# Optimization experiments

Measured on AMD Instinct MI355X. Metric: run time of the kernel, lower is better.

## Reference

```python
import jax, jax.numpy as jnp
import numpy as np

NUM_HEADS = 16
WINDOW = 16  # hard-coded in module; half-window = 8


def sliding_mask(seq_len):
    # mask[i, j] = 0 if j in [i - W//2, i + W//2], else -inf  (additive)
    i = jnp.arange(seq_len)[:, None]
    j = jnp.arange(seq_len)[None, :]
    return jnp.where(jnp.abs(i - j) <= WINDOW // 2, 0.0, -jnp.inf).astype(jnp.float32)


def setup_inputs() -> dict:
    key = jax.random.key(0)
    k1, k2, k3 = jax.random.split(key, 3)
    B, S, D = 2, 2048, 1024
    scale = 1.0 / np.sqrt(D)
    return {
        "input_embeddings": jax.random.normal(k1, (B, S, D), dtype=jnp.float32),
        "token_ids": jax.random.randint(k2, (B, S), 0, 32000, dtype=jnp.int64),
        # nn.MultiheadAttention params: packed in_proj [3D, D] + bias, out_proj [D, D] + bias
        "w_qkv": jax.random.normal(jax.random.fold_in(k3, 0), (3 * D, D), dtype=jnp.float32) * scale,
        "b_qkv": jnp.zeros((3 * D,), dtype=jnp.float32),
        "w_out": jax.random.normal(jax.random.fold_in(k3, 1), (D, D), dtype=jnp.float32) * scale,
        "b_out": jnp.zeros((D,), dtype=jnp.float32),
    }


def reference(input_embeddings, token_ids, w_qkv, b_qkv, w_out, b_out):
    B, S, D = input_embeddings.shape
    H = NUM_HEADS
    hd = D // H
    # packed QKV projection (torch in_proj): [B, S, 3D]
    qkv = input_embeddings @ w_qkv.T + b_qkv
    q, k, v = jnp.split(qkv, 3, axis=-1)
    # [B, H, S, hd]
    q = q.reshape(B, S, H, hd).transpose(0, 2, 1, 3)
    k = k.reshape(B, S, H, hd).transpose(0, 2, 1, 3)
    v = v.reshape(B, S, H, hd).transpose(0, 2, 1, 3)
    scores = jnp.einsum("bhqd,bhkd->bhqk", q, k) / jnp.sqrt(jnp.asarray(hd, q.dtype))
    scores = scores + sliding_mask(S)  # broadcast additive [S, S] mask
    attn = jax.nn.softmax(scores, axis=-1)
    ctx = jnp.einsum("bhqk,bhkd->bhqd", attn, v)
    ctx = ctx.transpose(0, 2, 1, 3).reshape(B, S, D)
    return ctx @ w_out.T + b_out
```

## Files before the change

### kernel.cpp

```cpp
#include <hip/hip_runtime.h>
#include <stdint.h>


typedef __bf16 bf16_t;
typedef bf16_t bf16x8 __attribute__((ext_vector_type(8)));
typedef unsigned short u16x8 __attribute__((ext_vector_type(8)));
typedef float f32x4 __attribute__((ext_vector_type(4)));

#define GLD16(g, l)                                                        \
  __builtin_amdgcn_global_load_lds(                                        \
      (const __attribute__((address_space(1))) void*)(g),                  \
      (__attribute__((address_space(3))) void*)(l), 16, 0, 0)

__device__ __forceinline__ unsigned short f2bf(float f) {
  unsigned int u = __float_as_uint(f);
  u += 0x7FFFu + ((u >> 16) & 1u);
  return (unsigned short)(u >> 16);
}

__device__ __forceinline__ bf16x8 ld16(const unsigned short* p) {
  return __builtin_bit_cast(bf16x8, *reinterpret_cast<const u16x8*>(p));
}

__global__ void cvt_all(const float* __restrict__ x, const float* __restrict__ wq,
                        const float* __restrict__ wo, unsigned short* __restrict__ xb,
                        unsigned short* __restrict__ wqb,
                        unsigned short* __restrict__ wob) {
  const int N0 = 1048576, N1 = 786432, N2 = 262144;
  for (int i = blockIdx.x * blockDim.x + threadIdx.x; i < N0 + N1 + N2;
       i += gridDim.x * blockDim.x) {
    const float4* src;
    unsigned short* dst;
    int j;
    if (i < N0) { src = (const float4*)x; dst = xb; j = i; }
    else if (i < N0 + N1) { src = (const float4*)wq; dst = wqb; j = i - N0; }
    else { src = (const float4*)wo; dst = wob; j = i - N0 - N1; }
    const float4 f = src[j];
    ushort4 o;
    o.x = f2bf(f.x); o.y = f2bf(f.y); o.z = f2bf(f.z); o.w = f2bf(f.w);
    reinterpret_cast<ushort4*>(dst)[j] = o;
  }
}

template <int EPI>
__global__ __launch_bounds__(256, 2) void gemm_bt(
    const unsigned short* __restrict__ A,
    const unsigned short* __restrict__ Bt,
    const float* __restrict__ bias,
    unsigned short* __restrict__ Cq, unsigned short* __restrict__ Ck,
    unsigned short* __restrict__ Cv, float* __restrict__ Cp, int M, int N,
    int K, int gny) {
  __shared__ unsigned short sA[2][8192];
  __shared__ unsigned short sB[2][8192];

  const int tid = threadIdx.x;
  const int wave = tid >> 6;
  const int lane = tid & 63;

  const int nwg = gridDim.x;
  const int bid = blockIdx.x;
  const int cw = (nwg >> 3) / gny;
  const int xcd = bid & 7;
  const int idx = bid >> 3;
  const int m0 = (xcd * cw + idx % cw) * 128;
  const int n0 = (idx / cw) * 128;

  const int wr = wave >> 1;
  const int wc = wave & 1;

  f32x4 acc[4][4] = {};

  const int srow = (wave << 3) + (lane >> 3);
  const int sslot = ((lane & 7) ^ (lane >> 3)) << 3;
  const unsigned short* Ag = A + (size_t)(m0 + srow) * K + sslot;
  const unsigned short* Bg = Bt + (size_t)(n0 + srow) * K + sslot;
  const int wdst = wave * 512;

  const int T = K >> 6;

  auto stage = [&](int t, int b) {
#pragma unroll
    for (int r = 0; r < 4; ++r) {
      GLD16(Ag + (size_t)(r * 32) * K + t * 64, &sA[b][r * 2048 + wdst]);
      GLD16(Bg + (size_t)(r * 32) * K + t * 64, &sB[b][r * 2048 + wdst]);
    }
  };

  stage(0, 0);
  stage(1, 1);

  const int kg = lane >> 4;
  const int l7 = lane & 7;
  const int arr = wr * 64 + (lane & 15);
  const int brr = wc * 64 + (lane & 15);

  for (int t = 0; t < T; ++t) {
    if (t < T - 1)
      asm volatile("s_waitcnt vmcnt(8)" ::: "memory");
    else
      asm volatile("s_waitcnt vmcnt(0)" ::: "memory");
    __builtin_amdgcn_s_barrier();

    const int b = t & 1;
    const unsigned short* sAb = sA[b];
    const unsigned short* sBb = sB[b];
    bf16x8 af[2][4], bfr[2][4];
#pragma unroll
    for (int st = 0; st < 2; ++st) {
#pragma unroll
      for (int f = 0; f < 4; ++f) {
        const int se = ((st << 2) | kg) ^ l7;
        af[st][f] = ld16(&sAb[(arr + f * 16) * 64 + (se << 3)]);
        bfr[st][f] = ld16(&sBb[(brr + f * 16) * 64 + (se << 3)]);
      }
    }
    asm volatile("s_waitcnt lgkmcnt(0)" ::: "memory");
    __builtin_amdgcn_sched_barrier(0);
    __builtin_amdgcn_s_barrier();

    if (t + 2 < T) stage(t + 2, b);

#pragma unroll
    for (int st = 0; st < 2; ++st)
#pragma unroll
      for (int i = 0; i < 4; ++i)
#pragma unroll
        for (int j = 0; j < 4; ++j)
          acc[i][j] = __builtin_amdgcn_mfma_f32_16x16x32_bf16(
              af[st][i], bfr[st][j], acc[i][j], 0, 0, 0);
  }

#pragma unroll
  for (int i = 0; i < 4; ++i) {
    const int row0 = m0 + wr * 64 + i * 16 + ((lane >> 4) << 2);
#pragma unroll
    for (int j = 0; j < 4; ++j) {
      const int col = n0 + wc * 64 + j * 16 + (lane & 15);
      const float bb = bias[col];
#pragma unroll
      for (int r = 0; r < 4; ++r) {
        const int m = row0 + r;
        const float val = acc[i][j][r] + bb;
        if (EPI == 0) {
          Cp[(size_t)m * N + col] = val;
        } else {
          const int b2 = m >> 11, s = m & 2047;
          const int which = col >> 10, nn = col & 1023;
          const int h = nn >> 6, d = nn & 63;
          const int bh = (b2 << 4) + h;
          const unsigned short vb = f2bf(val);
          if (which == 0)
            Cq[((size_t)(bh * 2048 + s)) * 64 + d] = vb;
          else if (which == 1)
            Ck[((size_t)(bh * 2048 + s)) * 64 + d] = vb;
          else
            Cv[((size_t)(bh * 64 + d)) * 2048 + s] = vb;
        }
      }
    }
  }
}

__global__ __launch_bounds__(256) void attn_mfma(
    const unsigned short* __restrict__ Qb, const unsigned short* __restrict__ Kb,
    const unsigned short* __restrict__ Vt, unsigned short* __restrict__ ctx) {
  __shared__ unsigned short P[4][16][40];
  const int wave = threadIdx.x >> 6;
  const int lane = threadIdx.x & 63;
  const int gw = (blockIdx.x << 2) + wave;
  const int bh = gw >> 7;
  const int i0 = (gw & 127) << 4;
  const int qr = lane & 15;
  const int kg = lane >> 4;
  const int kc = kg << 3;

  const size_t qbase = ((size_t)(bh * 2048 + i0 + qr)) * 64;
  const bf16x8 aq0 = ld16(Qb + qbase + kc);
  const bf16x8 aq1 = ld16(Qb + qbase + 32 + kc);

  f32x4 sc0 = {0.f, 0.f, 0.f, 0.f}, sc1 = {0.f, 0.f, 0.f, 0.f};
  {
    const int ka0 = i0 - 8 + qr;
    const int ka1 = ka0 + 16;
    const int kcl0 = min(max(ka0, 0), 2047);
    const int kcl1 = min(max(ka1, 0), 2047);
    const unsigned short* K0 = Kb + ((size_t)(bh * 2048 + kcl0)) * 64;
    const unsigned short* K1 = Kb + ((size_t)(bh * 2048 + kcl1)) * 64;
    sc0 = __builtin_amdgcn_mfma_f32_16x16x32_bf16(aq0, ld16(K0 + kc), sc0, 0, 0, 0);
    sc0 = __builtin_amdgcn_mfma_f32_16x16x32_bf16(aq1, ld16(K0 + 32 + kc), sc0, 0, 0, 0);
    sc1 = __builtin_amdgcn_mfma_f32_16x16x32_bf16(aq0, ld16(K1 + kc), sc1, 0, 0, 0);
    sc1 = __builtin_amdgcn_mfma_f32_16x16x32_bf16(aq1, ld16(K1 + 32 + kc), sc1, 0, 0, 0);
  }

  unsigned short* Pw = &P[wave][0][0];
  float lsum[4];
#pragma unroll
  for (int r = 0; r < 4; ++r) {
    const int q = (kg << 2) + r;
    const int key0 = qr, key1 = 16 + qr;
    const int ka0 = i0 - 8 + key0, ka1 = i0 - 8 + key1;
    const bool v0 = (q <= key0) && (key0 <= q + 16) && (ka0 >= 0) && (ka0 < 2048);
    const bool v1 = (q <= key1) && (key1 <= q + 16) && (ka1 >= 0) && (ka1 < 2048);
    const float e0 = v0 ? __expf(sc0[r] * 0.125f) : 0.f;
    const float e1 = v1 ? __expf(sc1[r] * 0.125f) : 0.f;
    Pw[q * 40 + key0] = f2bf(e0);
    Pw[q * 40 + key1] = f2bf(e1);
    float s = e0 + e1;
#pragma unroll
    for (int off = 1; off < 16; off <<= 1) s += __shfl_xor(s, off);
    lsum[r] = s;
  }

  const bf16x8 pa = ld16(&Pw[qr * 40 + kc]);

  const int base_s = min(max(i0 - 8 + kc, 0), 2040);
  f32x4 o[4];
  const f32x4 zero = {0.f, 0.f, 0.f, 0.f};
#pragma unroll
  for (int t2 = 0; t2 < 4; ++t2) {
    const unsigned short* Vr =
        Vt + ((size_t)(bh * 64 + t2 * 16 + qr)) * 2048 + base_s;
    o[t2] = __builtin_amdgcn_mfma_f32_16x16x32_bf16(pa, ld16(Vr), zero, 0, 0, 0);
  }

  const int b = bh >> 4, h = bh & 15;
  float rinv[4];
#pragma unroll
  for (int r = 0; r < 4; ++r) rinv[r] = 1.0f / lsum[r];
#pragma unroll
  for (int t2 = 0; t2 < 4; ++t2) {
#pragma unroll
    for (int r = 0; r < 4; ++r) {
      const int q = (kg << 2) + r;
      const int d = t2 * 16 + qr;
      ctx[((size_t)(b * 2048 + i0 + q)) * 1024 + (h << 6) + d] =
          f2bf(o[t2][r] * rinv[r]);
    }
  }
}

extern "C" void kernel_launch(void* const* d_in, const int* in_sizes, int n_in,
                              void* d_out, int out_size, void* d_ws,
                              size_t ws_size, hipStream_t stream) {
  const float* x = (const float*)d_in[0];
  const float* w_qkv = (const float*)d_in[2];
  const float* b_qkv = (const float*)d_in[3];
  const float* w_out = (const float*)d_in[4];
  const float* b_out = (const float*)d_in[5];
  float* out = (float*)d_out;

  char* ws = (char*)d_ws;
  unsigned short* xb    = (unsigned short*)(ws + 0);
  unsigned short* wqkvb = (unsigned short*)(ws + 8388608);
  unsigned short* woutb = (unsigned short*)(ws + 14680064);
  unsigned short* Qb    = (unsigned short*)(ws + 16777216);
  unsigned short* Kb    = (unsigned short*)(ws + 25165824);
  unsigned short* Vt    = (unsigned short*)(ws + 33554432);
  unsigned short* ctxb  = (unsigned short*)(ws + 41943040);

  cvt_all<<<2048, 256, 0, stream>>>(x, w_qkv, w_out, xb, wqkvb, woutb);

  gemm_bt<1><<<768, 256, 0, stream>>>(xb, wqkvb, b_qkv, Qb, Kb, Vt, nullptr,
                                      4096, 3072, 1024, 24);

  attn_mfma<<<1024, 256, 0, stream>>>(Qb, Kb, Vt, ctxb);

  gemm_bt<0><<<256, 256, 0, stream>>>(ctxb, woutb, b_out, nullptr, nullptr,
                                      nullptr, out, 4096, 1024, 1024, 8);
}
```

Measured before the change: 80.62 us.

## Replace QKV GEMM with 256x256-tile 512-thread kernel with prioritized MFMA

Adds a dedicated QKV projection kernel that uses 256x256 output tiles, 8 waves per block, and a double-buffered LDS pipeline built on direct global-to-LDS loads and explicit waitcnt/barrier scheduling. Each wave computes a 128x64 sub-tile, which raises arithmetic intensity per LDS byte, and s_setprio wraps the MFMA bursts. The generic gemm_bt is left as the fp32 output projection only. The cost is 192 blocks on a 256-CU device, so some CUs sit idle, plus 128 KB of LDS per block and much higher register pressure, which limits occupancy.

```diff
diff --git a/kernel.cpp b/kernel.cpp
--- a/kernel.cpp
+++ b/kernel.cpp
@@ -42,14 +42,137 @@
   }
 }
 
-template <int EPI>
+__global__ __launch_bounds__(512, 2) void gemm256_qkv(
+    const unsigned short* __restrict__ A,
+    const unsigned short* __restrict__ Bt,
+    const float* __restrict__ bias,
+    unsigned short* __restrict__ Cq, unsigned short* __restrict__ Ck,
+    unsigned short* __restrict__ Cv) {
+  __shared__ unsigned short sA[2][16384];
+  __shared__ unsigned short sB[2][16384];
+
+  const int K = 1024;
+  const int tid = threadIdx.x;
+  const int wave = tid >> 6;
+  const int lane = tid & 63;
+  const int bid = blockIdx.x;
+  const int m0 = (bid & 15) << 8;
+  const int n0 = (bid >> 4) << 8;
+
+  const int wr = wave >> 2;
+  const int wc = wave & 3;
+
+  f32x4 acc[8][4] = {};
+
+  const int srow8 = (wave << 3) + (lane >> 3);
+  const int sslot = ((lane & 7) ^ (lane >> 3)) << 3;
+  const unsigned short* Ag = A + (size_t)(m0 + srow8) * K + sslot;
+  const unsigned short* Bg = Bt + (size_t)(n0 + srow8) * K + sslot;
+  const int wdst = wave * 512;
+
+  const int T = 16;
+
+  auto stage = [&](int t, int b) {
+#pragma unroll
+    for (int h = 0; h < 2; ++h)
+#pragma unroll
+      for (int r = 0; r < 2; ++r) {
+        const size_t go = (size_t)(h * 128 + r * 64) * K + t * 64;
+        const int lo = h * 8192 + r * 4096 + wdst;
+        GLD16(Ag + go, &sA[b][lo]);
+        GLD16(Bg + go, &sB[b][lo]);
+      }
+  };
+
+  stage(0, 0);
+  stage(1, 1);
+
+  const int kg = lane >> 4;
+  const int l7 = lane & 7;
+  const int a0 = wr * 8192 + (lane & 15) * 64 + ((kg ^ l7) << 3);
+  const int b0 =
+      (wc >> 1) * 8192 + ((wc & 1) * 64 + (lane & 15)) * 64 + ((kg ^ l7) << 3);
+
+  for (int t = 0; t < T; ++t) {
+    if (t < T - 1)
+      asm volatile("s_waitcnt vmcnt(8)" ::: "memory");
+    else
+      asm volatile("s_waitcnt vmcnt(0)" ::: "memory");
+    __builtin_amdgcn_s_barrier();
+
+    const int b = t & 1;
+    const unsigned short* sAb = sA[b];
+    const unsigned short* sBb = sB[b];
+
+    bf16x8 af[8], bf[4];
+#pragma unroll
+    for (int m = 0; m < 8; ++m) af[m] = ld16(&sAb[a0 + m * 1024]);
+#pragma unroll
+    for (int n = 0; n < 4; ++n) bf[n] = ld16(&sBb[b0 + n * 1024]);
+    asm volatile("s_waitcnt lgkmcnt(0)" ::: "memory");
+    __builtin_amdgcn_sched_barrier(0);
+    __builtin_amdgcn_s_setprio(1);
+#pragma unroll
+    for (int m = 0; m < 8; ++m)
+#pragma unroll
+      for (int n = 0; n < 4; ++n)
+        acc[m][n] = __builtin_amdgcn_mfma_f32_16x16x32_bf16(af[m], bf[n],
+                                                            acc[m][n], 0, 0, 0);
+    __builtin_amdgcn_s_setprio(0);
+
+    bf16x8 af1[8], bf1[4];
+#pragma unroll
+    for (int m = 0; m < 8; ++m) af1[m] = ld16(&sAb[(a0 ^ 32) + m * 1024]);
+#pragma unroll
+    for (int n = 0; n < 4; ++n) bf1[n] = ld16(&sBb[(b0 ^ 32) + n * 1024]);
+    asm volatile("s_waitcnt lgkmcnt(0)" ::: "memory");
+    __builtin_amdgcn_sched_barrier(0);
+    __builtin_amdgcn_s_barrier();
+
+    if (t + 2 < T) stage(t + 2, b);
+
+    __builtin_amdgcn_s_setprio(1);
+#pragma unroll
+    for (int m = 0; m < 8; ++m)
+#pragma unroll
+      for (int n = 0; n < 4; ++n)
+        acc[m][n] = __builtin_amdgcn_mfma_f32_16x16x32_bf16(af1[m], bf1[n],
+                                                            acc[m][n], 0, 0, 0);
+    __builtin_amdgcn_s_setprio(0);
+  }
+
+#pragma unroll
+  for (int m = 0; m < 8; ++m) {
+    const int row0 = m0 + wr * 128 + m * 16 + ((lane >> 4) << 2);
+#pragma unroll
+    for (int n = 0; n < 4; ++n) {
+      const int col = n0 + wc * 64 + n * 16 + (lane & 15);
+      const float bb = bias[col];
+#pragma unroll
+      for (int r = 0; r < 4; ++r) {
+        const int mm = row0 + r;
+        const float val = acc[m][n][r] + bb;
+        const int b2 = mm >> 11, s = mm & 2047;
+        const int which = col >> 10, nn = col & 1023;
+        const int h = nn >> 6, d = nn & 63;
+        const int bh = (b2 << 4) + h;
+        const unsigned short vb = f2bf(val);
+        if (which == 0)
+          Cq[((size_t)(bh * 2048 + s)) * 64 + d] = vb;
+        else if (which == 1)
+          Ck[((size_t)(bh * 2048 + s)) * 64 + d] = vb;
+        else
+          Cv[((size_t)(bh * 64 + d)) * 2048 + s] = vb;
+      }
+    }
+  }
+}
+
 __global__ __launch_bounds__(256, 2) void gemm_bt(
     const unsigned short* __restrict__ A,
     const unsigned short* __restrict__ Bt,
     const float* __restrict__ bias,
-    unsigned short* __restrict__ Cq, unsigned short* __restrict__ Ck,
-    unsigned short* __restrict__ Cv, float* __restrict__ Cp, int M, int N,
-    int K, int gny) {
+    float* __restrict__ Cp, int M, int N, int K, int gny) {
   __shared__ unsigned short sA[2][8192];
   __shared__ unsigned short sB[2][8192];
 
@@ -138,25 +261,8 @@
       const int col = n0 + wc * 64 + j * 16 + (lane & 15);
       const float bb = bias[col];
 #pragma unroll
-      for (int r = 0; r < 4; ++r) {
-        const int m = row0 + r;
-        const float val = acc[i][j][r] + bb;
-        if (EPI == 0) {
-          Cp[(size_t)m * N + col] = val;
-        } else {
-          const int b2 = m >> 11, s = m & 2047;
-          const int which = col >> 10, nn = col & 1023;
-          const int h = nn >> 6, d = nn & 63;
-          const int bh = (b2 << 4) + h;
-          const unsigned short vb = f2bf(val);
-          if (which == 0)
-            Cq[((size_t)(bh * 2048 + s)) * 64 + d] = vb;
-          else if (which == 1)
-            Ck[((size_t)(bh * 2048 + s)) * 64 + d] = vb;
-          else
-            Cv[((size_t)(bh * 64 + d)) * 2048 + s] = vb;
-        }
-      }
+      for (int r = 0; r < 4; ++r)
+        Cp[(size_t)(row0 + r) * N + col] = acc[i][j][r] + bb;
     }
   }
 }
@@ -260,11 +366,9 @@
 
   cvt_all<<<2048, 256, 0, stream>>>(x, w_qkv, w_out, xb, wqkvb, woutb);
 
-  gemm_bt<1><<<768, 256, 0, stream>>>(xb, wqkvb, b_qkv, Qb, Kb, Vt, nullptr,
-                                      4096, 3072, 1024, 24);
+  gemm256_qkv<<<192, 512, 0, stream>>>(xb, wqkvb, b_qkv, Qb, Kb, Vt);
 
   attn_mfma<<<1024, 256, 0, stream>>>(Qb, Kb, Vt, ctxb);
 
-  gemm_bt<0><<<256, 256, 0, stream>>>(ctxb, woutb, b_out, nullptr, nullptr,
-                                      nullptr, out, 4096, 1024, 1024, 8);
-}
+  gemm_bt<<<256, 256, 0, stream>>>(ctxb, woutb, b_out, out, 4096, 1024, 1024, 8);
+}
```

After: 94.98 us. +17.8%, slower.

## Add dedicated QKV GEMM kernel with triple-buffered BK=32 LDS pipeline

Applied to the files above, without the earlier changes.

Replaces the templated GEMM for the QKV projection with a dedicated kernel that uses a 3-stage LDS ring of 32-wide K tiles loaded by global_load_lds, with explicit vmcnt waits, XOR-swizzled LDS slots and s_setprio around the MFMA block. It also drops the XCD-aware block remapping in favour of a plain 2D grid and removes the occupancy hint. The aim is to hide global load latency better through deeper prefetch with less LDS per block. The cost is more barriers per K step and the loss of L2 locality from the XCD mapping.

```diff
diff --git a/kernel.cpp b/kernel.cpp
--- a/kernel.cpp
+++ b/kernel.cpp
@@ -42,14 +42,118 @@
   }
 }
 
-template <int EPI>
+__global__ __launch_bounds__(256) void gemm_qkv(
+    const unsigned short* __restrict__ A,
+    const unsigned short* __restrict__ Bt,
+    const float* __restrict__ bias,
+    unsigned short* __restrict__ Cq, unsigned short* __restrict__ Ck,
+    unsigned short* __restrict__ Cv) {
+  __shared__ unsigned short sA[3][4096];
+  __shared__ unsigned short sB[3][4096];
+
+  const int K = 1024;
+  const int tid = threadIdx.x;
+  const int wave = tid >> 6;
+  const int lane = tid & 63;
+  const int m0 = blockIdx.x << 7;
+  const int n0 = blockIdx.y << 7;
+
+  const int wr = wave >> 1;
+  const int wc = wave & 1;
+
+  f32x4 acc[4][4] = {};
+
+  const int srow = (wave << 4) + (lane >> 2);
+  const int sslot = (((lane & 3) ^ ((lane >> 3) & 3)) << 3);
+  const unsigned short* Ag = A + (size_t)(m0 + srow) * K + sslot;
+  const unsigned short* Bg = Bt + (size_t)(n0 + srow) * K + sslot;
+  const int wdst = wave * 512;
+
+  auto stage = [&](int t, int b) {
+#pragma unroll
+    for (int r = 0; r < 2; ++r) {
+      GLD16(Ag + (size_t)(r * 64) * K + t * 32, &sA[b][r * 2048 + wdst]);
+      GLD16(Bg + (size_t)(r * 64) * K + t * 32, &sB[b][r * 2048 + wdst]);
+    }
+  };
+
+  stage(0, 0);
+  stage(1, 1);
+  stage(2, 2);
+
+  const int qr = lane & 15;
+  const int kg = lane >> 4;
+  const int geff8 = ((kg ^ ((qr >> 1) & 3)) << 3);
+  const int ar = wr * 64 + qr;
+  const int br = wc * 64 + qr;
+
+  for (int t = 0; t < 32; ++t) {
+    if (t < 30)
+      asm volatile("s_waitcnt vmcnt(8)" ::: "memory");
+    else if (t == 30)
+      asm volatile("s_waitcnt vmcnt(4)" ::: "memory");
+    else
+      asm volatile("s_waitcnt vmcnt(0)" ::: "memory");
+    __builtin_amdgcn_s_barrier();
+
+    const int b = t % 3;
+    const unsigned short* sAb = sA[b];
+    const unsigned short* sBb = sB[b];
+
+    bf16x8 af[4], bf[4];
+#pragma unroll
+    for (int f = 0; f < 4; ++f) {
+      af[f] = ld16(&sAb[(ar + f * 16) * 32 + geff8]);
+      bf[f] = ld16(&sBb[(br + f * 16) * 32 + geff8]);
+    }
+    asm volatile("s_waitcnt lgkmcnt(0)" ::: "memory");
+    __builtin_amdgcn_sched_barrier(0);
+    __builtin_amdgcn_s_barrier();
+
+    if (t + 3 < 32) stage(t + 3, b);
+
+    __builtin_amdgcn_s_setprio(1);
+#pragma unroll
+    for (int i = 0; i < 4; ++i)
+#pragma unroll
+      for (int j = 0; j < 4; ++j)
+        acc[i][j] = __builtin_amdgcn_mfma_f32_16x16x32_bf16(af[i], bf[j],
+                                                            acc[i][j], 0, 0, 0);
+    __builtin_amdgcn_s_setprio(0);
+  }
+
+#pragma unroll
+  for (int i = 0; i < 4; ++i) {
+    const int row0 = m0 + wr * 64 + i * 16 + ((lane >> 4) << 2);
+#pragma unroll
+    for (int j = 0; j < 4; ++j) {
+      const int col = n0 + wc * 64 + j * 16 + (lane & 15);
+      const float bb = bias[col];
+#pragma unroll
+      for (int r = 0; r < 4; ++r) {
+        const int mm = row0 + r;
+        const float val = acc[i][j][r] + bb;
+        const int b2 = mm >> 11, s = mm & 2047;
+        const int which = col >> 10, nn = col & 1023;
+        const int h = nn >> 6, d = nn & 63;
+        const int bh = (b2 << 4) + h;
+        const unsigned short vb = f2bf(val);
+        if (which == 0)
+          Cq[((size_t)(bh * 2048 + s)) * 64 + d] = vb;
+        else if (which == 1)
+          Ck[((size_t)(bh * 2048 + s)) * 64 + d] = vb;
+        else
+          Cv[((size_t)(bh * 64 + d)) * 2048 + s] = vb;
+      }
+    }
+  }
+}
+
 __global__ __launch_bounds__(256, 2) void gemm_bt(
     const unsigned short* __restrict__ A,
     const unsigned short* __restrict__ Bt,
     const float* __restrict__ bias,
-    unsigned short* __restrict__ Cq, unsigned short* __restrict__ Ck,
-    unsigned short* __restrict__ Cv, float* __restrict__ Cp, int M, int N,
-    int K, int gny) {
+    float* __restrict__ Cp, int M, int N, int K, int gny) {
   __shared__ unsigned short sA[2][8192];
   __shared__ unsigned short sB[2][8192];
 
@@ -138,25 +242,8 @@
       const int col = n0 + wc * 64 + j * 16 + (lane & 15);
       const float bb = bias[col];
 #pragma unroll
-      for (int r = 0; r < 4; ++r) {
-        const int m = row0 + r;
-        const float val = acc[i][j][r] + bb;
-        if (EPI == 0) {
-          Cp[(size_t)m * N + col] = val;
-        } else {
-          const int b2 = m >> 11, s = m & 2047;
-          const int which = col >> 10, nn = col & 1023;
-          const int h = nn >> 6, d = nn & 63;
-          const int bh = (b2 << 4) + h;
-          const unsigned short vb = f2bf(val);
-          if (which == 0)
-            Cq[((size_t)(bh * 2048 + s)) * 64 + d] = vb;
-          else if (which == 1)
-            Ck[((size_t)(bh * 2048 + s)) * 64 + d] = vb;
-          else
-            Cv[((size_t)(bh * 64 + d)) * 2048 + s] = vb;
-        }
-      }
+      for (int r = 0; r < 4; ++r)
+        Cp[(size_t)(row0 + r) * N + col] = acc[i][j][r] + bb;
     }
   }
 }
@@ -260,11 +347,9 @@
 
   cvt_all<<<2048, 256, 0, stream>>>(x, w_qkv, w_out, xb, wqkvb, woutb);
 
-  gemm_bt<1><<<768, 256, 0, stream>>>(xb, wqkvb, b_qkv, Qb, Kb, Vt, nullptr,
-                                      4096, 3072, 1024, 24);
+  gemm_qkv<<<dim3(32, 24), 256, 0, stream>>>(xb, wqkvb, b_qkv, Qb, Kb, Vt);
 
   attn_mfma<<<1024, 256, 0, stream>>>(Qb, Kb, Vt, ctxb);
 
-  gemm_bt<0><<<256, 256, 0, stream>>>(ctxb, woutb, b_out, nullptr, nullptr,
-                                      nullptr, out, 4096, 1024, 1024, 8);
-}
+  gemm_bt<<<256, 256, 0, stream>>>(ctxb, woutb, b_out, out, 4096, 1024, 1024, 8);
+}
```

After: 79.21 us. Within noise of the previous version (-1.8%).
